# Performance work log

Hardware: AMD Instinct MI355X
Metric: run time of the kernel (lower is better)

Reference implementation:

```python
import jax, jax.numpy as jnp
import numpy as np

NUM_SPECIES = 4
NUM_PAIRS = NUM_SPECIES * (NUM_SPECIES + 1) // 2  # 10 species pairs
RCR = 5.2   # radial cutoff (Angstrom)
RCA = 3.5   # angular cutoff (must be < RCR)
ETA_R = 16.0
SHF_R = jnp.asarray(0.9 + 0.26875 * np.arange(16), dtype=jnp.float32)
ETA_A = 8.0
ZETA = 32.0
SHF_A = jnp.asarray(0.9 + 0.65 * np.arange(4), dtype=jnp.float32)       # 4 angular radial shifts
SHF_Z = jnp.asarray((np.pi / 16.0) * (1.0 + 2.0 * np.arange(8)), dtype=jnp.float32)  # 8 angle sections


def _triu_index(num_species):
    # mirrors AEVComputer._calculate_triu_index
    s1, s2 = np.triu_indices(num_species, 0)
    ret = np.zeros((num_species, num_species), dtype=np.int32)
    ret[s1, s2] = np.arange(len(s1))
    ret[s2, s1] = np.arange(len(s1))
    return jnp.asarray(ret)

TRIU = _triu_index(NUM_SPECIES)


def _fc(d, rc):
    # cosine cutoff; the (d <= rc) validity is applied via masks outside
    return 0.5 * jnp.cos(jnp.pi * d / rc) + 0.5


def _aev(species, coords):
    N, A = species.shape
    dt = coords.dtype
    diff = coords[:, None, :, :] - coords[:, :, None, :]          # (N,i,j,3): r_j - r_i
    eye = jnp.eye(A, dtype=bool)
    d2 = jnp.sum(diff * diff, axis=-1)
    dist = jnp.sqrt(jnp.where(eye, 1.0, d2))                      # (N,i,j), self-distance guarded

    # ---- radial AEV: 0.25 * exp(-EtaR*(d-ShfR)^2) * fc(d), scattered by neighbor species ----
    rmask = (~eye) & (dist <= RCR)
    rad = 0.25 * jnp.exp(-ETA_R * (dist[..., None] - SHF_R) ** 2) * _fc(dist, RCR)[..., None]
    rad = rad * rmask[..., None].astype(dt)                       # (N,i,j,16)
    sp1h = jax.nn.one_hot(species, NUM_SPECIES, dtype=dt)         # (N,j,S)
    radial_aev = jnp.einsum('nijr,njs->nisr', rad, sp1h).reshape(N, A, -1)  # (N,A,64)

    # ---- angular AEV over triples (i; j,k), j,k neighbors of i within RCA ----
    amask = (~eye) & (dist <= RCA)                                # (N,i,j)
    tri = amask[:, :, :, None] & amask[:, :, None, :] & (~eye)[None, None]  # (N,i,j,k), j!=k
    dot = jnp.einsum('nijc,nikc->nijk', diff, diff)
    cos = 0.95 * dot / (dist[:, :, :, None] * dist[:, :, None, :])  # 0.95 stabilizer as in torchani
    theta = jnp.arccos(jnp.clip(cos, -0.95, 0.95))                # (N,i,j,k)
    fcj = _fc(dist, RCA)
    base = 2.0 * fcj[:, :, :, None] * fcj[:, :, None, :] * tri.astype(dt)
    davg = 0.5 * (dist[:, :, :, None] + dist[:, :, None, :])
    f2 = jnp.exp(-ETA_A * (davg[..., None] - SHF_A) ** 2)         # (N,i,j,k,ShfA=4)
    f1 = ((1.0 + jnp.cos(theta[..., None] - SHF_Z)) * 0.5) ** ZETA  # (N,i,j,k,ShfZ=8)
    term = (base[..., None, None] * f2[..., :, None] * f1[..., None, :]).reshape(N, A, A, A, -1)
    pair_idx = TRIU[species[:, :, None], species[:, None, :]]     # (N,j,k)
    pair1h = jax.nn.one_hot(pair_idx, NUM_PAIRS, dtype=dt)        # (N,j,k,P=10)
    # each unordered pair {j,k} is counted once in torchani -> 0.5 * symmetric ordered sum
    angular_aev = 0.5 * jnp.einsum('nijkq,njkp->nipq', term, pair1h).reshape(N, A, -1)  # (N,A,320)

    return jnp.concatenate([radial_aev, angular_aev], axis=-1)    # (N,A,384)


def setup_inputs():
    key = jax.random.key(0)
    k1, k2 = jax.random.split(key)
    N, A, BOX = 16, 64, 12.0
    coords = jax.random.uniform(k1, (N, A, 3), dtype=jnp.float32) * BOX  # atoms in a 12 A box
    species = jax.random.randint(k2, (N, A), 0, NUM_SPECIES)
    return {"species": species, "coords": coords}


def reference(species, coords):
    # SpeciesAEV: (species, aev) with aev shape (N, A, aev_length=384)
    return species, _aev(species, coords)
```

## Files before the change

kernel.cpp:

```cpp
#include <hip/hip_runtime.h>

#define RCR 5.2f
#define RCA 3.5f
#define PI_F 3.14159265358979323846f

__global__ __launch_bounds__(64) void aev_kernel(
    const int* __restrict__ species,
    const float* __restrict__ coords,
    float* __restrict__ out,
    int NA)
{
    const int blk = blockIdx.x;
    const int n   = blk >> 6;
    const int i   = blk & 63;
    const int tid = threadIdx.x;

    __shared__ float sx[64], sy[64], sz[64];
    __shared__ int   ssp[64];
    __shared__ float dxs[64], dys[64], dzs[64], ds[64];
    __shared__ float pre_r[64];
    __shared__ float fca[64];
    __shared__ int   nbr[64];
    __shared__ int   rnbr[64];
    __shared__ float s_ang[320];

    const float* c = coords + (size_t)(n * 64) * 3;
    sx[tid]  = c[tid * 3 + 0];
    sy[tid]  = c[tid * 3 + 1];
    sz[tid]  = c[tid * 3 + 2];
    ssp[tid] = species[n * 64 + tid];
    __syncthreads();

    const float xi = sx[i], yi = sy[i], zi = sz[i];
    const float ddx = sx[tid] - xi;
    const float ddy = sy[tid] - yi;
    const float ddz = sz[tid] - zi;
    const float d   = sqrtf(ddx * ddx + ddy * ddy + ddz * ddz);
    dxs[tid] = ddx; dys[tid] = ddy; dzs[tid] = ddz; ds[tid] = d;

    const bool isj = (tid != i);
    pre_r[tid] = 0.25f * (0.5f * __cosf((PI_F / RCR) * d) + 0.5f);
    fca[tid]   = 0.5f * __cosf((PI_F / RCA) * d) + 0.5f;

    const bool rpred = isj && (d <= RCR);
    const unsigned long long rbal = __ballot(rpred);
    if (rpred) {
        const int pos = __popcll(rbal & ((1ull << tid) - 1ull));
        rnbr[pos] = tid;
    }
    const int MR = __popcll(rbal);

    const bool apred = isj && (d <= RCA);
    const unsigned long long bal = __ballot(apred);
    if (apred) {
        const int pos = __popcll(bal & ((1ull << tid) - 1ull));
        nbr[pos] = tid;
    }
    const int M = __popcll(bal);

    for (int f = tid; f < 320; f += 64) s_ang[f] = 0.0f;
    __syncthreads();

    const int   my_s   = tid >> 4;
    const float my_shf = 0.9f + 0.26875f * (float)(tid & 15);
    float racc = 0.0f;
    #pragma unroll 4
    for (int jj = 0; jj < MR; jj++) {
        const int j = rnbr[jj];
        const float t = ds[j] - my_shf;
        racc += (ssp[j] == my_s) ? pre_r[j] * __expf(-16.0f * t * t) : 0.0f;
    }

    const float CPHI[8] = { 0.98078528f,  0.83146961f,  0.55557023f,  0.19509032f,
                           -0.19509032f, -0.55557023f, -0.83146961f, -0.98078528f};
    const float SPHI[8] = { 0.19509032f,  0.55557023f,  0.83146961f,  0.98078528f,
                            0.98078528f,  0.83146961f,  0.55557023f,  0.19509032f};
    const float SHFA[4] = {0.9f, 1.55f, 2.2f, 2.85f};

    const int P = (M * (M - 1)) >> 1;
    for (int q = tid; q < P; q += 64) {
        int jj = (int)((1.0f + sqrtf(1.0f + 8.0f * (float)q)) * 0.5f);
        while (((jj * (jj - 1)) >> 1) > q) --jj;
        while ((((jj + 1) * jj) >> 1) <= q) ++jj;
        const int kk = q - ((jj * (jj - 1)) >> 1);

        const int j = nbr[jj], k = nbr[kk];
        const float dij = ds[j], dik = ds[k];
        const float dot = dxs[j] * dxs[k] + dys[j] * dys[k] + dzs[j] * dzs[k];
        float cosv = 0.95f * dot * __builtin_amdgcn_rcpf(dij * dik);
        cosv = fminf(0.95f, fmaxf(-0.95f, cosv));
        const float sinv = sqrtf(fmaxf(0.0f, 1.0f - cosv * cosv));
        const float base2 = 2.0f * fca[j] * fca[k];
        const float davg  = 0.5f * (dij + dik);
        const int s1 = ssp[j], s2 = ssp[k];
        const int smin = (s1 < s2) ? s1 : s2;
        const int smax = (s1 < s2) ? s2 : s1;
        const int pidx = ((smin * (7 - smin)) >> 1) + smax;

        float f2[4];
        #pragma unroll
        for (int a = 0; a < 4; a++) {
            const float t = davg - SHFA[a];
            f2[a] = base2 * __expf(-8.0f * t * t);
        }
        float t32z[8];
        #pragma unroll
        for (int z = 0; z < 8; z++) {
            const float w  = 0.5f + 0.5f * (cosv * CPHI[z] + sinv * SPHI[z]);
            const float t2 = w * w, t4 = t2 * t2, t8 = t4 * t4, t16 = t8 * t8;
            t32z[z] = t16 * t16;
        }
        float* dst = &s_ang[pidx * 32];
        #pragma unroll
        for (int a = 0; a < 4; a++)
            #pragma unroll
            for (int z = 0; z < 8; z++)
                atomicAdd(&dst[a * 8 + z], f2[a] * t32z[z]);
    }
    __syncthreads();

    const int atom = n * 64 + i;
    if (tid == 0) out[atom] = (float)ssp[i];
    float* dstg = out + NA + (size_t)atom * 384;
    dstg[tid] = racc;
    #pragma unroll
    for (int u = 0; u < 5; u++) dstg[64 + tid + 64 * u] = s_ang[tid + 64 * u];
}

extern "C" void kernel_launch(void* const* d_in, const int* in_sizes, int n_in,
                              void* d_out, int out_size, void* d_ws, size_t ws_size,
                              hipStream_t stream) {
    const int*   species = (const int*)d_in[0];
    const float* coords  = (const float*)d_in[1];
    float*       out     = (float*)d_out;
    const int NA = in_sizes[0];
    aev_kernel<<<NA, 64, 0, stream>>>(species, coords, out, NA);
}
```

Measured before the change: 63.51 us.

## Split radial and angular work across two waves with species-bucketed compacted neighbor lists

Each block now launches two waves instead of one. Wave 0 builds per-species compacted radial neighbor lists and computes the radial AEV, while wave 1 runs the angular triple loop concurrently. The angular neighbor data (displacements, distances, cutoffs, species) is compacted directly into contiguous shared arrays, so the double indirection through neighbor indices goes away. The radial loop also no longer iterates over neighbors of the wrong species. In exchange the block uses more threads, and the angular work still runs on a single wave, so any speedup is limited to overlapping the radial and angular phases.

After: 62.15 us. 1.02x faster.

```diff
diff --git a/kernel.cpp b/kernel.cpp
--- a/kernel.cpp
+++ b/kernel.cpp
@@ -4,127 +4,137 @@
 #define RCA 3.5f
 #define PI_F 3.14159265358979323846f
 
-__global__ __launch_bounds__(64) void aev_kernel(
+__global__ __launch_bounds__(128) void aev_kernel(
     const int* __restrict__ species,
     const float* __restrict__ coords,
     float* __restrict__ out,
     int NA)
 {
-    const int blk = blockIdx.x;
-    const int n   = blk >> 6;
-    const int i   = blk & 63;
-    const int tid = threadIdx.x;
+    const int blk  = blockIdx.x;
+    const int n    = blk >> 6;
+    const int i    = blk & 63;
+    const int tid  = threadIdx.x;
+    const int lane = tid & 63;
+    const int wave = tid >> 6;
 
     __shared__ float sx[64], sy[64], sz[64];
     __shared__ int   ssp[64];
-    __shared__ float dxs[64], dys[64], dzs[64], ds[64];
-    __shared__ float pre_r[64];
-    __shared__ float fca[64];
-    __shared__ int   nbr[64];
-    __shared__ int   rnbr[64];
+    __shared__ float adx[64], ady[64], adz[64], ads[64], afc[64];
+    __shared__ int   asp[64];
+    __shared__ float rds[4][65], rpre[4][65];
+    __shared__ int   cnts[5];
     __shared__ float s_ang[320];
 
-    const float* c = coords + (size_t)(n * 64) * 3;
-    sx[tid]  = c[tid * 3 + 0];
-    sy[tid]  = c[tid * 3 + 1];
-    sz[tid]  = c[tid * 3 + 2];
-    ssp[tid] = species[n * 64 + tid];
+    if (tid < 64) {
+        const float* c = coords + (size_t)(n * 64) * 3;
+        sx[tid]  = c[tid * 3 + 0];
+        sy[tid]  = c[tid * 3 + 1];
+        sz[tid]  = c[tid * 3 + 2];
+        ssp[tid] = species[n * 64 + tid];
+    }
+    for (int f = tid; f < 320; f += 128) s_ang[f] = 0.0f;
     __syncthreads();
 
-    const float xi = sx[i], yi = sy[i], zi = sz[i];
-    const float ddx = sx[tid] - xi;
-    const float ddy = sy[tid] - yi;
-    const float ddz = sz[tid] - zi;
-    const float d   = sqrtf(ddx * ddx + ddy * ddy + ddz * ddz);
-    dxs[tid] = ddx; dys[tid] = ddy; dzs[tid] = ddz; ds[tid] = d;
+    if (wave == 0) {
+        const float xi  = sx[i], yi = sy[i], zi = sz[i];
+        const float ddx = sx[lane] - xi;
+        const float ddy = sy[lane] - yi;
+        const float ddz = sz[lane] - zi;
+        const float d   = sqrtf(ddx * ddx + ddy * ddy + ddz * ddz);
+        const bool  isj = (lane != i);
+        const int   sp  = ssp[lane];
+        const float pre = 0.25f * (0.5f * __cosf((PI_F / RCR) * d) + 0.5f);
+        const float fcv = 0.5f * __cosf((PI_F / RCA) * d) + 0.5f;
 
-    const bool isj = (tid != i);
-    pre_r[tid] = 0.25f * (0.5f * __cosf((PI_F / RCR) * d) + 0.5f);
-    fca[tid]   = 0.5f * __cosf((PI_F / RCA) * d) + 0.5f;
+        const bool rpred = isj && (d <= RCR);
+        #pragma unroll
+        for (int s = 0; s < 4; s++) {
+            const bool p = rpred && (sp == s);
+            const unsigned long long b = __ballot(p);
+            if (p) {
+                const int pos = __popcll(b & ((1ull << lane) - 1ull));
+                rds[s][pos]  = d;
+                rpre[s][pos] = pre;
+            }
+            if (lane == 0) cnts[s] = __popcll(b);
+        }
 
-    const bool rpred = isj && (d <= RCR);
-    const unsigned long long rbal = __ballot(rpred);
-    if (rpred) {
-        const int pos = __popcll(rbal & ((1ull << tid) - 1ull));
-        rnbr[pos] = tid;
+        const bool apred = isj && (d <= RCA);
+        const unsigned long long b = __ballot(apred);
+        if (apred) {
+            const int pos = __popcll(b & ((1ull << lane) - 1ull));
+            adx[pos] = ddx; ady[pos] = ddy; adz[pos] = ddz;
+            ads[pos] = d;   afc[pos] = fcv; asp[pos] = sp;
+        }
+        if (lane == 0) cnts[4] = __popcll(b);
     }
-    const int MR = __popcll(rbal);
-
-    const bool apred = isj && (d <= RCA);
-    const unsigned long long bal = __ballot(apred);
-    if (apred) {
-        const int pos = __popcll(bal & ((1ull << tid) - 1ull));
-        nbr[pos] = tid;
-    }
-    const int M = __popcll(bal);
-
-    for (int f = tid; f < 320; f += 64) s_ang[f] = 0.0f;
     __syncthreads();
 
-    const int   my_s   = tid >> 4;
-    const float my_shf = 0.9f + 0.26875f * (float)(tid & 15);
     float racc = 0.0f;
-    #pragma unroll 4
-    for (int jj = 0; jj < MR; jj++) {
-        const int j = rnbr[jj];
-        const float t = ds[j] - my_shf;
-        racc += (ssp[j] == my_s) ? pre_r[j] * __expf(-16.0f * t * t) : 0.0f;
-    }
+    if (wave == 0) {
+        const int   s   = lane >> 4;
+        const float shf = 0.9f + 0.26875f * (float)(lane & 15);
+        const int   mr  = cnts[s];
+        #pragma unroll 4
+        for (int jj = 0; jj < mr; jj++) {
+            const float t = rds[s][jj] - shf;
+            racc += rpre[s][jj] * __expf(-16.0f * t * t);
+        }
+    } else {
+        const float CPHI[8] = { 0.98078528f,  0.83146961f,  0.55557023f,  0.19509032f,
+                               -0.19509032f, -0.55557023f, -0.83146961f, -0.98078528f};
+        const float SPHI[8] = { 0.19509032f,  0.55557023f,  0.83146961f,  0.98078528f,
+                                0.98078528f,  0.83146961f,  0.55557023f,  0.19509032f};
+        const float SHFA[4] = {0.9f, 1.55f, 2.2f, 2.85f};
 
-    const float CPHI[8] = { 0.98078528f,  0.83146961f,  0.55557023f,  0.19509032f,
-                           -0.19509032f, -0.55557023f, -0.83146961f, -0.98078528f};
-    const float SPHI[8] = { 0.19509032f,  0.55557023f,  0.83146961f,  0.98078528f,
-                            0.98078528f,  0.83146961f,  0.55557023f,  0.19509032f};
-    const float SHFA[4] = {0.9f, 1.55f, 2.2f, 2.85f};
+        const int M = cnts[4];
+        const int P = (M * (M - 1)) >> 1;
+        for (int q = lane; q < P; q += 64) {
+            int jj = (int)((1.0f + sqrtf(1.0f + 8.0f * (float)q)) * 0.5f);
+            while (((jj * (jj - 1)) >> 1) > q) --jj;
+            while ((((jj + 1) * jj) >> 1) <= q) ++jj;
+            const int kk = q - ((jj * (jj - 1)) >> 1);
 
-    const int P = (M * (M - 1)) >> 1;
-    for (int q = tid; q < P; q += 64) {
-        int jj = (int)((1.0f + sqrtf(1.0f + 8.0f * (float)q)) * 0.5f);
-        while (((jj * (jj - 1)) >> 1) > q) --jj;
-        while ((((jj + 1) * jj) >> 1) <= q) ++jj;
-        const int kk = q - ((jj * (jj - 1)) >> 1);
+            const float dij = ads[jj], dik = ads[kk];
+            const float dot = adx[jj] * adx[kk] + ady[jj] * ady[kk] + adz[jj] * adz[kk];
+            float cosv = 0.95f * dot * __builtin_amdgcn_rcpf(dij * dik);
+            cosv = fminf(0.95f, fmaxf(-0.95f, cosv));
+            const float sinv  = sqrtf(fmaxf(0.0f, 1.0f - cosv * cosv));
+            const float base2 = 2.0f * afc[jj] * afc[kk];
+            const float davg  = 0.5f * (dij + dik);
+            const int s1 = asp[jj], s2 = asp[kk];
+            const int smin = (s1 < s2) ? s1 : s2;
+            const int smax = (s1 < s2) ? s2 : s1;
+            const int pidx = ((smin * (7 - smin)) >> 1) + smax;
 
-        const int j = nbr[jj], k = nbr[kk];
-        const float dij = ds[j], dik = ds[k];
-        const float dot = dxs[j] * dxs[k] + dys[j] * dys[k] + dzs[j] * dzs[k];
-        float cosv = 0.95f * dot * __builtin_amdgcn_rcpf(dij * dik);
-        cosv = fminf(0.95f, fmaxf(-0.95f, cosv));
-        const float sinv = sqrtf(fmaxf(0.0f, 1.0f - cosv * cosv));
-        const float base2 = 2.0f * fca[j] * fca[k];
-        const float davg  = 0.5f * (dij + dik);
-        const int s1 = ssp[j], s2 = ssp[k];
-        const int smin = (s1 < s2) ? s1 : s2;
-        const int smax = (s1 < s2) ? s2 : s1;
-        const int pidx = ((smin * (7 - smin)) >> 1) + smax;
-
-        float f2[4];
-        #pragma unroll
-        for (int a = 0; a < 4; a++) {
-            const float t = davg - SHFA[a];
-            f2[a] = base2 * __expf(-8.0f * t * t);
+            float f2[4];
+            #pragma unroll
+            for (int a = 0; a < 4; a++) {
+                const float t = davg - SHFA[a];
+                f2[a] = base2 * __expf(-8.0f * t * t);
+            }
+            float t32z[8];
+            #pragma unroll
+            for (int z = 0; z < 8; z++) {
+                const float w  = 0.5f + 0.5f * (cosv * CPHI[z] + sinv * SPHI[z]);
+                const float t2 = w * w, t4 = t2 * t2, t8 = t4 * t4, t16 = t8 * t8;
+                t32z[z] = t16 * t16;
+            }
+            float* dst = &s_ang[pidx * 32];
+            #pragma unroll
+            for (int a = 0; a < 4; a++)
+                #pragma unroll
+                for (int z = 0; z < 8; z++)
+                    atomicAdd(&dst[a * 8 + z], f2[a] * t32z[z]);
         }
-        float t32z[8];
-        #pragma unroll
-        for (int z = 0; z < 8; z++) {
-            const float w  = 0.5f + 0.5f * (cosv * CPHI[z] + sinv * SPHI[z]);
-            const float t2 = w * w, t4 = t2 * t2, t8 = t4 * t4, t16 = t8 * t8;
-            t32z[z] = t16 * t16;
-        }
-        float* dst = &s_ang[pidx * 32];
-        #pragma unroll
-        for (int a = 0; a < 4; a++)
-            #pragma unroll
-            for (int z = 0; z < 8; z++)
-                atomicAdd(&dst[a * 8 + z], f2[a] * t32z[z]);
     }
     __syncthreads();
 
     const int atom = n * 64 + i;
     if (tid == 0) out[atom] = (float)ssp[i];
     float* dstg = out + NA + (size_t)atom * 384;
-    dstg[tid] = racc;
-    #pragma unroll
-    for (int u = 0; u < 5; u++) dstg[64 + tid + 64 * u] = s_ang[tid + 64 * u];
+    if (wave == 0) dstg[lane] = racc;
+    for (int u = tid; u < 320; u += 128) dstg[64 + u] = s_ang[u];
 }
 
 extern "C" void kernel_launch(void* const* d_in, const int* in_sizes, int n_in,
@@ -134,5 +144,5 @@
     const float* coords  = (const float*)d_in[1];
     float*       out     = (float*)d_out;
     const int NA = in_sizes[0];
-    aev_kernel<<<NA, 64, 0, stream>>>(species, coords, out, NA);
+    aev_kernel<<<NA, 128, 0, stream>>>(species, coords, out, NA);
 }
```
